# Performance work log

Measured on AMD Instinct MI355X. Metric: run time of the kernel, lower is better.

Reference implementation:

```python
import jax, jax.numpy as jnp
import numpy as np

B, S, D, H = 2, 2048, 1024, 16
HD = D // H  # head_dim = 64
ROPE_BASE = 10000.0
NEG = -1e9


def rope_cos_sin(seq_len, head_dim, dtype):
    inv_freq = 1.0 / (ROPE_BASE ** (jnp.arange(0, head_dim, 2, dtype=jnp.float32) / head_dim))
    t = jnp.arange(seq_len, dtype=jnp.float32)
    freqs = jnp.outer(t, inv_freq)              # [S, HD/2]
    emb = jnp.concatenate([freqs, freqs], axis=-1)  # [S, HD]
    return jnp.cos(emb).astype(dtype), jnp.sin(emb).astype(dtype)


def rotate_half(x):
    half = x.shape[-1] // 2
    return jnp.concatenate([-x[..., half:], x[..., :half]], axis=-1)


def setup_inputs() -> dict:
    key = jax.random.key(0)
    ks = jax.random.split(key, 9)
    s = 0.02
    x = jax.random.normal(ks[0], (B, S, D), dtype=jnp.float32)
    # additive causal mask: 0 on/below diagonal, -1e9 above
    mask = jnp.where(jnp.tril(jnp.ones((S, S), dtype=bool)), 0.0, NEG).astype(jnp.float32)
    params = {
        'Wq': jax.random.normal(ks[1], (D, D), jnp.float32) * s,
        'bq': jnp.zeros((D,), jnp.float32),
        'Wk': jax.random.normal(ks[2], (D, D), jnp.float32) * s,
        'bk': jnp.zeros((D,), jnp.float32),
        'Wv': jax.random.normal(ks[3], (D, D), jnp.float32) * s,
        'bv': jnp.zeros((D,), jnp.float32),
        'Wo': jax.random.normal(ks[4], (D, D), jnp.float32) * s,
        'bo': jnp.zeros((D,), jnp.float32),
    }
    return {'x': x, 'mask': mask, **params}


def reference(x, mask, Wq, bq, Wk, bk, Wv, bv, Wo, bo):
    Bv, Sv, Dv = x.shape
    q = (x @ Wq + bq).reshape(Bv, Sv, H, HD).transpose(0, 2, 1, 3)  # [B,H,S,HD]
    k = (x @ Wk + bk).reshape(Bv, Sv, H, HD).transpose(0, 2, 1, 3)
    v = (x @ Wv + bv).reshape(Bv, Sv, H, HD).transpose(0, 2, 1, 3)
    cos, sin = rope_cos_sin(Sv, HD, x.dtype)      # [S, HD]
    cos = cos[None, None]                          # [1,1,S,HD]
    sin = sin[None, None]
    q = q * cos + rotate_half(q) * sin
    k = k * cos + rotate_half(k) * sin
    scale = jnp.asarray(np.sqrt(HD), x.dtype)
    scores = jnp.einsum('bhqd,bhkd->bhqk', q, k) / scale  # [B,H,S,S]
    scores = scores + mask[None, None]
    attn = jax.nn.softmax(scores, axis=-1)
    out = jnp.einsum('bhqk,bhkd->bhqd', attn, v)   # [B,H,S,HD]
    out = out.transpose(0, 2, 1, 3).reshape(Bv, Sv, Dv)
    return out @ Wo + bo
```

## Files before the change

kernel.cpp:

```cpp
#include <hip/hip_runtime.h>
#include <hip/hip_bf16.h>
#include <cstdint>

typedef __bf16 bf16;
typedef __bf16 bf16x4 __attribute__((ext_vector_type(4)));
typedef __bf16 bf16x8 __attribute__((ext_vector_type(8)));
typedef float f32x4 __attribute__((ext_vector_type(4)));

#define DEV __device__ __forceinline__

DEV void gl_lds16(const void* g, void* l) {
    __builtin_amdgcn_global_load_lds(
        (__attribute__((address_space(1))) void*)(uintptr_t)g,
        (__attribute__((address_space(3))) void*)(uint32_t)(uintptr_t)l,
        16, 0, 0);
}

DEV f32x4 mfma16(bf16x8 a, bf16x8 b, f32x4 c) {
    return __builtin_amdgcn_mfma_f32_16x16x32_bf16(a, b, c, 0, 0, 0);
}

__global__ __launch_bounds__(256) void prep_k(
    const float* __restrict__ x, bf16* __restrict__ xb,
    const float* __restrict__ w0, const float* __restrict__ w1,
    const float* __restrict__ w2, const float* __restrict__ w3,
    bf16* __restrict__ WT, float* __restrict__ cosT, float* __restrict__ sinT) {
    __shared__ float t[32][33];
    const int blk = (int)blockIdx.x;
    const int tid = threadIdx.x;
    if (blk < 4096) {
        const int i = blk * 256 + tid;
        const float4 v = ((const float4*)x)[i];
        bf16x4 o = {(bf16)v.x, (bf16)v.y, (bf16)v.z, (bf16)v.w};
        *(bf16x4*)(xb + (size_t)i * 4) = o;
    } else if (blk < 8192) {
        const int j = blk - 4096;
        const int z = j >> 10, jy = (j >> 5) & 31, jx = j & 31;
        const float* W = z == 0 ? w0 : z == 1 ? w1 : z == 2 ? w2 : w3;
        bf16* dst = WT + (size_t)z * 1024 * 1024;
        const int tx = tid & 31, ty = tid >> 5;
        const int kb = jx * 32, nb = jy * 32;
#pragma unroll
        for (int i = 0; i < 4; ++i)
            t[ty + i * 8][tx] = W[(size_t)(kb + ty + i * 8) * 1024 + nb + tx];
        __syncthreads();
#pragma unroll
        for (int i = 0; i < 4; ++i)
            dst[(size_t)(nb + ty + i * 8) * 1024 + kb + tx] = (bf16)t[tx][ty + i * 8];
    } else {
        const int tt = (blk - 8192) * 256 + tid;
        const int s = tt >> 6, i = tt & 31;
        const float inv = expf(-(float)i * (9.210340371976184f / 32.0f));
        const float ang = (float)s * inv;
        cosT[tt] = cosf(ang);
        sinT[tt] = sinf(ang);
    }
}

__global__ __launch_bounds__(512, 1) void gemm256_k(
    const bf16* __restrict__ A, const bf16* __restrict__ BT,
    const float* __restrict__ bq, const float* __restrict__ bk,
    const float* __restrict__ bv,
    bf16* __restrict__ outQ, bf16* __restrict__ outK, bf16* __restrict__ outV,
    const float* __restrict__ cosT, const float* __restrict__ sinT) {
    extern __shared__ char smem[];
    const int tid = threadIdx.x;
    const int lane = tid & 63, wv = tid >> 6;
    const int wm2 = wv >> 2, wn2 = wv & 3;
    const int q = lane & 15, g = lane >> 4;

    const int gid = (int)blockIdx.x;
    const int xcd = gid & 7, idx = gid >> 3;
    const int bm = (xcd & 3) * 4 + (idx & 3);
    const int bn = (xcd >> 2) * 6 + (idx >> 2);

    const bf16* Ab = A + (size_t)bm * 256 * 1024;
    const bf16* Bb = BT + (size_t)bn * 256 * 1024;

    auto stage = [&](int b, int kb) {
        char* base = smem + b * 65536;
#pragma unroll
        for (int i = 0; i < 4; ++i) {
            const int Xs = i * 8192 + tid * 16;
            const int row = Xs >> 7;
            const int cb = (Xs & 127) ^ ((row & 7) << 4);
            gl_lds16(Ab + (size_t)row * 1024 + kb + (cb >> 1), base + Xs);
        }
#pragma unroll
        for (int i = 0; i < 4; ++i) {
            const int Xs = i * 8192 + tid * 16;
            const int row = Xs >> 7;
            const int cb = (Xs & 127) ^ ((row & 7) << 4);
            gl_lds16(Bb + (size_t)row * 1024 + kb + (cb >> 1), base + 32768 + Xs);
        }
    };

    f32x4 acc[8][4] = {};

    stage(0, 0);

    for (int t = 0; t < 16; ++t) {
        asm volatile("s_waitcnt vmcnt(0)" ::: "memory");
        __builtin_amdgcn_s_barrier();
        if (t + 1 < 16) stage((t + 1) & 1, (t + 1) * 64);
        const char* cbuf = smem + (t & 1) * 65536;
        bf16x8 bfr[4];
#pragma unroll
        for (int p = 0; p < 4; ++p) {
            const int ks = p >> 1, mih = p & 1;
            if (mih == 0) {
#pragma unroll
                for (int ni = 0; ni < 4; ++ni) {
                    const int row = wn2 * 64 + ni * 16 + q;
                    bfr[ni] = *(const bf16x8*)(cbuf + 32768 + row * 128 +
                                               ((ks * 64 + g * 16) ^ ((q & 7) << 4)));
                }
            }
            bf16x8 af[4];
#pragma unroll
            for (int j = 0; j < 4; ++j) {
                const int row = wm2 * 128 + (mih * 4 + j) * 16 + q;
                af[j] = *(const bf16x8*)(cbuf + row * 128 +
                                         ((ks * 64 + g * 16) ^ ((q & 7) << 4)));
            }
            __builtin_amdgcn_s_setprio(1);
#pragma unroll
            for (int j = 0; j < 4; ++j)
#pragma unroll
                for (int ni = 0; ni < 4; ++ni)
                    acc[mih * 4 + j][ni] = mfma16(af[j], bfr[ni], acc[mih * 4 + j][ni]);
            __builtin_amdgcn_s_setprio(0);
        }
    }

    const int n0 = bn * 256 + wn2 * 64;
    const int seg = n0 >> 10;
    const int nloc = n0 & 1023;
    const int h = nloc >> 6;
    const float* bias = seg == 0 ? bq : (seg == 1 ? bk : bv);
    const float qsc = (seg == 0) ? 0.125f : 1.0f;
    float bvv[4];
#pragma unroll
    for (int ni = 0; ni < 4; ++ni) bvv[ni] = bias[nloc + ni * 16 + q];

    if (seg < 2) {
        bf16* dst = seg == 0 ? outQ : outK;
#pragma unroll
        for (int mi = 0; mi < 8; ++mi) {
#pragma unroll
            for (int r = 0; r < 4; ++r) {
                const int m = bm * 256 + wm2 * 128 + mi * 16 + g * 4 + r;
                const int s = m & 2047, bb = m >> 11;
                const size_t rowb = ((size_t)((bb << 4) | h) * 2048 + s) * 64;
#pragma unroll
                for (int ni = 0; ni < 4; ++ni) {
                    const int hd = ni * 16 + q;
                    const float c = cosT[s * 64 + hd], sn = sinT[s * 64 + hd];
                    const float v0 = acc[mi][ni][r] + bvv[ni];
                    const float v1 = acc[mi][ni ^ 2][r] + bvv[ni ^ 2];
                    dst[rowb + hd] = (bf16)((v0 * c + (ni < 2 ? -v1 : v1) * sn) * qsc);
                }
            }
        }
    } else {
        __builtin_amdgcn_s_barrier();
        bf16* Tw = (bf16*)smem + wv * (64 * 72);
        const int bb = (bm * 256) >> 11;
        bf16* vbase = outV + (size_t)((bb << 4) | h) * (64 * 2048);
#pragma unroll
        for (int sh = 0; sh < 2; ++sh) {
#pragma unroll
            for (int mi2 = 0; mi2 < 4; ++mi2)
#pragma unroll
                for (int ni = 0; ni < 4; ++ni)
#pragma unroll
                    for (int r = 0; r < 4; ++r)
                        Tw[(ni * 16 + q) * 72 + mi2 * 16 + g * 4 + r] =
                            (bf16)(acc[sh * 4 + mi2][ni][r] + bvv[ni]);
            const int s0 = ((bm * 256) & 2047) + wm2 * 128 + sh * 64;
#pragma unroll
            for (int i = 0; i < 8; ++i) {
                const int row = i * 8 + (lane >> 3);
                const int col = (lane & 7) * 8;
                bf16x8 vvv = *(const bf16x8*)(Tw + row * 72 + col);
                *(bf16x8*)(vbase + (size_t)row * 2048 + s0 + col) = vvv;
            }
        }
    }
}

__global__ __launch_bounds__(256) void gemmo_k(
    const bf16* __restrict__ A, const bf16* __restrict__ BT,
    const float* __restrict__ bias0, float* __restrict__ outF) {
    extern __shared__ char smem[];
    const int tid = threadIdx.x;
    const int lane = tid & 63;
    const int wv = tid >> 6;
    const int wm = wv >> 1, wn = wv & 1;
    const int bm = blockIdx.x, bn = blockIdx.y;
    const int q = lane & 15, g = lane >> 4;

    const bf16* Ab = A + (size_t)bm * 128 * 1024;
    const bf16* Bb = BT + (size_t)bn * 128 * 1024;
    const int r0 = tid >> 2, c0 = (tid & 3) * 8;

    auto stage = [&](int b, int kb) {
        char* base = smem + b * 16384;
        gl_lds16(Ab + (size_t)r0 * 1024 + kb + c0, base + tid * 16);
        gl_lds16(Ab + (size_t)(r0 + 64) * 1024 + kb + c0, base + 4096 + tid * 16);
        gl_lds16(Bb + (size_t)r0 * 1024 + kb + c0, base + 8192 + tid * 16);
        gl_lds16(Bb + (size_t)(r0 + 64) * 1024 + kb + c0, base + 12288 + tid * 16);
    };

    f32x4 acc[4][4] = {};

    stage(0, 0);
    stage(1, 32);
    asm volatile("s_waitcnt vmcnt(4)" ::: "memory");
    __builtin_amdgcn_s_barrier();

    for (int kt = 0; kt < 32; ++kt) {
        if (kt + 2 < 32) stage((kt + 2) % 3, (kt + 2) * 32);
        const bf16* As = (const bf16*)(smem + (kt % 3) * 16384);
        const bf16* Bs = As + 128 * 32;
        bf16x8 af[4], bfr[4];
#pragma unroll
        for (int mi = 0; mi < 4; ++mi)
            af[mi] = *(const bf16x8*)(As + (wm * 64 + mi * 16 + q) * 32 + g * 8);
#pragma unroll
        for (int ni = 0; ni < 4; ++ni)
            bfr[ni] = *(const bf16x8*)(Bs + (wn * 64 + ni * 16 + q) * 32 + g * 8);
#pragma unroll
        for (int mi = 0; mi < 4; ++mi)
#pragma unroll
            for (int ni = 0; ni < 4; ++ni)
                acc[mi][ni] = mfma16(af[mi], bfr[ni], acc[mi][ni]);
        if (kt + 2 < 32) asm volatile("s_waitcnt vmcnt(4)" ::: "memory");
        else             asm volatile("s_waitcnt vmcnt(0)" ::: "memory");
        __builtin_amdgcn_s_barrier();
    }

    const int n0 = bn * 128 + wn * 64;
    float bvv[4];
#pragma unroll
    for (int ni = 0; ni < 4; ++ni) bvv[ni] = bias0[n0 + ni * 16 + q];
#pragma unroll
    for (int mi = 0; mi < 4; ++mi)
#pragma unroll
        for (int r = 0; r < 4; ++r) {
            const int m = bm * 128 + wm * 64 + mi * 16 + g * 4 + r;
#pragma unroll
            for (int ni = 0; ni < 4; ++ni)
                outF[(size_t)m * 1024 + n0 + ni * 16 + q] = acc[mi][ni][r] + bvv[ni];
        }
}

__global__ __launch_bounds__(512, 2) void attn_k(const bf16* __restrict__ Qr,
                                                 const bf16* __restrict__ Kr,
                                                 const bf16* __restrict__ Vt,
                                                 bf16* __restrict__ AO) {
    const int gid = (int)blockIdx.x;
    const int xcd = gid & 7;
    const int bh = xcd + 8 * ((gid >> 3) & 3);
    const int idx = gid >> 5;
    const int p = idx >> 1;
    const int h = 1 - (idx & 1);
    const int tid = threadIdx.x;
    const int lane = tid & 63, wv = tid >> 6;
    const int q = lane & 15, g = lane >> 4;
    const int qt_w = (wv >> 2) ? p : (15 - p);
    const int q0w = qt_w * 128 + h * 64 + (wv & 3) * 16;
    const int nt = 31 - 2 * p + h;
    const size_t hb = (size_t)bh * (2048 * 64);
    extern __shared__ char smem[];
    bf16* P = (bf16*)(smem + 49152 + wv * 2304);

    const bf16* Kg = Kr + hb;
    const bf16* Vg = Vt + hb;
    const int swz = (q & 7) << 4;

    auto stage = [&](int b, int kb) {
        char* base = smem + b * 16384;
        {
            const int X = tid * 16;
            const int row = X >> 7;
            const int cbg = (X & 127) ^ ((row & 7) << 4);
            gl_lds16(Kg + (size_t)(kb + row) * 64 + (cbg >> 1), base + X);
        }
        {
            const int X = tid * 16;
            const int row = X >> 7;
            const int cbg = (X & 127) ^ ((row & 7) << 4);
            gl_lds16(Vg + (size_t)row * 2048 + kb + (cbg >> 1), base + 8192 + X);
        }
    };

    bf16x8 qf[2];
    {
        const bf16* qp = Qr + hb + (size_t)(q0w + q) * 64 + g * 8;
        qf[0] = *(const bf16x8*)(qp);
        qf[1] = *(const bf16x8*)(qp + 32);
    }
    f32x4 o[4] = {};
    float l_run = 0.0f;
    const f32x4 z4 = {0.f, 0.f, 0.f, 0.f};
    const int rmax = q0w + 15;

    stage(0, 0);
    stage(1, 64);
    asm volatile("s_waitcnt vmcnt(2)" ::: "memory");
    __builtin_amdgcn_s_barrier();

    for (int kt = 0; kt < nt; ++kt) {
        const int kb = kt * 64;
        if (kt + 2 < nt) stage((kt + 2) % 3, kb + 128);
        if (kb <= rmax) {
            char* Kl = smem + (kt % 3) * 16384;
            char* Vl = Kl + 8192;
            f32x4 st[4];
            __builtin_amdgcn_s_setprio(1);
#pragma unroll
            for (int f = 0; f < 4; ++f) {
                const int row = f * 16 + q;
                const bf16x8 k0 = *(const bf16x8*)(Kl + row * 128 + ((g * 16) ^ swz));
                const bf16x8 k1 = *(const bf16x8*)(Kl + row * 128 + ((64 + g * 16) ^ swz));
                f32x4 t0 = mfma16(k0, qf[0], z4);
                st[f] = mfma16(k1, qf[1], t0);
            }
            __builtin_amdgcn_s_setprio(0);
            bf16x8 vf[4][2];
#pragma unroll
            for (int nf = 0; nf < 4; ++nf) {
                const int row = nf * 16 + q;
                vf[nf][0] = *(const bf16x8*)(Vl + row * 128 + ((g * 16) ^ swz));
                vf[nf][1] = *(const bf16x8*)(Vl + row * 128 + ((64 + g * 16) ^ swz));
            }
            float tsum = 0.f;
            if (kb + 63 > q0w) {
#pragma unroll
                for (int f = 0; f < 4; ++f)
#pragma unroll
                    for (int r = 0; r < 4; ++r) {
                        float sv = st[f][r];
                        if (kb + f * 16 + g * 4 + r > q0w + q) sv = -3.0e38f;
                        const float pv = __expf(fminf(sv, 20.0f));
                        st[f][r] = pv;
                        tsum += pv;
                    }
            } else {
#pragma unroll
                for (int f = 0; f < 4; ++f)
#pragma unroll
                    for (int r = 0; r < 4; ++r) {
                        const float pv = __expf(fminf(st[f][r], 20.0f));
                        st[f][r] = pv;
                        tsum += pv;
                    }
            }
            l_run += tsum;
#pragma unroll
            for (int f = 0; f < 4; ++f) {
                bf16x4 pv = {(bf16)st[f][0], (bf16)st[f][1],
                             (bf16)st[f][2], (bf16)st[f][3]};
                *(bf16x4*)&P[q * 72 + f * 16 + g * 4] = pv;
            }
            __builtin_amdgcn_s_setprio(1);
#pragma unroll
            for (int t = 0; t < 2; ++t) {
                const bf16x8 pa = *(const bf16x8*)&P[q * 72 + t * 32 + g * 8];
#pragma unroll
                for (int nf = 0; nf < 4; ++nf)
                    o[nf] = mfma16(pa, vf[nf][t], o[nf]);
            }
            __builtin_amdgcn_s_setprio(0);
        }
        if (kt + 2 < nt) asm volatile("s_waitcnt vmcnt(2)" ::: "memory");
        else             asm volatile("s_waitcnt vmcnt(0)" ::: "memory");
        __builtin_amdgcn_s_barrier();
    }

    l_run += __shfl_xor(l_run, 16);
    l_run += __shfl_xor(l_run, 32);
    float li[4];
#pragma unroll
    for (int r = 0; r < 4; ++r) li[r] = 1.0f / __shfl(l_run, g * 4 + r);
    const int b_ = bh >> 4, h_ = bh & 15;
#pragma unroll
    for (int nf = 0; nf < 4; ++nf)
#pragma unroll
        for (int r = 0; r < 4; ++r) {
            const int qg = q0w + g * 4 + r;
            AO[(size_t)(b_ * 2048 + qg) * 1024 + h_ * 64 + nf * 16 + q] =
                (bf16)(o[nf][r] * li[r]);
        }
}


extern "C" void kernel_launch(void* const* d_in, const int* in_sizes, int n_in,
                              void* d_out, int out_size, void* d_ws, size_t ws_size,
                              hipStream_t stream) {
    const float* x  = (const float*)d_in[0];
    const float* Wq = (const float*)d_in[2];
    const float* bq = (const float*)d_in[3];
    const float* Wk = (const float*)d_in[4];
    const float* bk = (const float*)d_in[5];
    const float* Wv = (const float*)d_in[6];
    const float* bv = (const float*)d_in[7];
    const float* Wo = (const float*)d_in[8];
    const float* bo = (const float*)d_in[9];
    float* out = (float*)d_out;
    char* ws = (char*)d_ws;
    const size_t MB_ = 1024 * 1024;
    bf16* xb    = (bf16*)(ws);
    bf16* WT    = (bf16*)(ws + 8 * MB_);
    bf16* Qrp   = (bf16*)(ws + 16 * MB_);
    bf16* Krp   = (bf16*)(ws + 24 * MB_);
    bf16* Vt    = (bf16*)(ws + 32 * MB_);
    bf16* AO    = (bf16*)(ws + 40 * MB_);
    float* cosT = (float*)(ws + 48 * MB_);
    float* sinT = (float*)(ws + 48 * MB_ + 512 * 1024);

    hipFuncSetAttribute((const void*)gemm256_k,
                        hipFuncAttributeMaxDynamicSharedMemorySize, 131072);

    prep_k<<<8704, 256, 0, stream>>>(x, xb, Wq, Wk, Wv, Wo, WT, cosT, sinT);
    gemm256_k<<<dim3(192), 512, 131072, stream>>>(xb, WT, bq, bk, bv,
                                                  Qrp, Krp, Vt, cosT, sinT);
    attn_k<<<dim3(512, 1), 512, 67584, stream>>>(Qrp, Krp, Vt, AO);
    gemmo_k<<<dim3(32, 8), 256, 49152, stream>>>(AO, WT + (size_t)3072 * 1024, bo, out);
}
```

Measured before the change: 97.30 us.

## Split KV tile across wave halves in attention and merge partial sums

The attention kernel now gives each block a single 64-row query tile, so the grid doubles to 1024 blocks. The two groups of four waves each process half of every 64-key tile and combine their partial outputs and row sums through shared memory at the end. This replaces the earlier pairing of a light and a heavy causal query tile per block, with the aim of more parallelism and less per-wave work per key tile. The cost is heavier load imbalance across blocks (ordered longest first), a shared-memory merge step with an extra barrier, and only half the waves doing the final writes.

```diff
diff --git a/kernel.cpp b/kernel.cpp
--- a/kernel.cpp
+++ b/kernel.cpp
@@ -262,18 +262,16 @@
     const int gid = (int)blockIdx.x;
     const int xcd = gid & 7;
     const int bh = xcd + 8 * ((gid >> 3) & 3);
-    const int idx = gid >> 5;
-    const int p = idx >> 1;
-    const int h = 1 - (idx & 1);
+    const int j = 31 - (gid >> 5);
     const int tid = threadIdx.x;
     const int lane = tid & 63, wv = tid >> 6;
     const int q = lane & 15, g = lane >> 4;
-    const int qt_w = (wv >> 2) ? p : (15 - p);
-    const int q0w = qt_w * 128 + h * 64 + (wv & 3) * 16;
-    const int nt = 31 - 2 * p + h;
+    const int half = wv >> 2;
+    const int q0w = j * 64 + (wv & 3) * 16;
+    const int nt = j + 1;
     const size_t hb = (size_t)bh * (2048 * 64);
     extern __shared__ char smem[];
-    bf16* P = (bf16*)(smem + 49152 + wv * 2304);
+    bf16* P = (bf16*)(smem + 49152 + wv * 1280);
 
     const bf16* Kg = Kr + hb;
     const bf16* Vg = Vt + hb;
@@ -307,49 +305,49 @@
     const int rmax = q0w + 15;
 
     stage(0, 0);
-    stage(1, 64);
+    if (nt > 1) stage(1, 64);
     asm volatile("s_waitcnt vmcnt(2)" ::: "memory");
     __builtin_amdgcn_s_barrier();
 
     for (int kt = 0; kt < nt; ++kt) {
         const int kb = kt * 64;
         if (kt + 2 < nt) stage((kt + 2) % 3, kb + 128);
-        if (kb <= rmax) {
+        const int kvb = kb + half * 32;
+        if (kvb <= rmax) {
             char* Kl = smem + (kt % 3) * 16384;
             char* Vl = Kl + 8192;
-            f32x4 st[4];
+            f32x4 st[2];
             __builtin_amdgcn_s_setprio(1);
 #pragma unroll
-            for (int f = 0; f < 4; ++f) {
-                const int row = f * 16 + q;
+            for (int f = 0; f < 2; ++f) {
+                const int row = half * 32 + f * 16 + q;
                 const bf16x8 k0 = *(const bf16x8*)(Kl + row * 128 + ((g * 16) ^ swz));
                 const bf16x8 k1 = *(const bf16x8*)(Kl + row * 128 + ((64 + g * 16) ^ swz));
                 f32x4 t0 = mfma16(k0, qf[0], z4);
                 st[f] = mfma16(k1, qf[1], t0);
             }
             __builtin_amdgcn_s_setprio(0);
-            bf16x8 vf[4][2];
+            bf16x8 vf[4];
 #pragma unroll
             for (int nf = 0; nf < 4; ++nf) {
                 const int row = nf * 16 + q;
-                vf[nf][0] = *(const bf16x8*)(Vl + row * 128 + ((g * 16) ^ swz));
-                vf[nf][1] = *(const bf16x8*)(Vl + row * 128 + ((64 + g * 16) ^ swz));
+                vf[nf] = *(const bf16x8*)(Vl + row * 128 + ((half * 64 + g * 16) ^ swz));
             }
             float tsum = 0.f;
-            if (kb + 63 > q0w) {
-#pragma unroll
-                for (int f = 0; f < 4; ++f)
+            if (kvb + 31 > q0w) {
+#pragma unroll
+                for (int f = 0; f < 2; ++f)
 #pragma unroll
                     for (int r = 0; r < 4; ++r) {
                         float sv = st[f][r];
-                        if (kb + f * 16 + g * 4 + r > q0w + q) sv = -3.0e38f;
+                        if (kvb + f * 16 + g * 4 + r > q0w + q) sv = -3.0e38f;
                         const float pv = __expf(fminf(sv, 20.0f));
                         st[f][r] = pv;
                         tsum += pv;
                     }
             } else {
 #pragma unroll
-                for (int f = 0; f < 4; ++f)
+                for (int f = 0; f < 2; ++f)
 #pragma unroll
                     for (int r = 0; r < 4; ++r) {
                         const float pv = __expf(fminf(st[f][r], 20.0f));
@@ -359,18 +357,17 @@
             }
             l_run += tsum;
 #pragma unroll
-            for (int f = 0; f < 4; ++f) {
+            for (int f = 0; f < 2; ++f) {
                 bf16x4 pv = {(bf16)st[f][0], (bf16)st[f][1],
                              (bf16)st[f][2], (bf16)st[f][3]};
-                *(bf16x4*)&P[q * 72 + f * 16 + g * 4] = pv;
+                *(bf16x4*)&P[q * 40 + f * 16 + g * 4] = pv;
             }
             __builtin_amdgcn_s_setprio(1);
-#pragma unroll
-            for (int t = 0; t < 2; ++t) {
-                const bf16x8 pa = *(const bf16x8*)&P[q * 72 + t * 32 + g * 8];
+            {
+                const bf16x8 pa = *(const bf16x8*)&P[q * 40 + g * 8];
 #pragma unroll
                 for (int nf = 0; nf < 4; ++nf)
-                    o[nf] = mfma16(pa, vf[nf][t], o[nf]);
+                    o[nf] = mfma16(pa, vf[nf], o[nf]);
             }
             __builtin_amdgcn_s_setprio(0);
         }
@@ -379,20 +376,36 @@
         __builtin_amdgcn_s_barrier();
     }
 
-    l_run += __shfl_xor(l_run, 16);
-    l_run += __shfl_xor(l_run, 32);
-    float li[4];
-#pragma unroll
-    for (int r = 0; r < 4; ++r) li[r] = 1.0f / __shfl(l_run, g * 4 + r);
-    const int b_ = bh >> 4, h_ = bh & 15;
-#pragma unroll
-    for (int nf = 0; nf < 4; ++nf)
-#pragma unroll
-        for (int r = 0; r < 4; ++r) {
-            const int qg = q0w + g * 4 + r;
-            AO[(size_t)(b_ * 2048 + qg) * 1024 + h_ * 64 + nf * 16 + q] =
-                (bf16)(o[nf][r] * li[r]);
-        }
+    float* mrg = (float*)(smem + (wv & 3) * 4352);
+    if (half) {
+#pragma unroll
+        for (int nf = 0; nf < 4; ++nf)
+#pragma unroll
+            for (int r = 0; r < 4; ++r) mrg[(nf * 4 + r) * 64 + lane] = o[nf][r];
+        mrg[16 * 64 + lane] = l_run;
+    }
+    __builtin_amdgcn_s_barrier();
+    if (!half) {
+#pragma unroll
+        for (int nf = 0; nf < 4; ++nf)
+#pragma unroll
+            for (int r = 0; r < 4; ++r) o[nf][r] += mrg[(nf * 4 + r) * 64 + lane];
+        l_run += mrg[16 * 64 + lane];
+        l_run += __shfl_xor(l_run, 16);
+        l_run += __shfl_xor(l_run, 32);
+        float li[4];
+#pragma unroll
+        for (int r = 0; r < 4; ++r) li[r] = 1.0f / __shfl(l_run, g * 4 + r);
+        const int b_ = bh >> 4, h_ = bh & 15;
+#pragma unroll
+        for (int nf = 0; nf < 4; ++nf)
+#pragma unroll
+            for (int r = 0; r < 4; ++r) {
+                const int qg = q0w + g * 4 + r;
+                AO[(size_t)(b_ * 2048 + qg) * 1024 + h_ * 64 + nf * 16 + q] =
+                    (bf16)(o[nf][r] * li[r]);
+            }
+    }
 }
 
 
@@ -426,6 +439,6 @@
     prep_k<<<8704, 256, 0, stream>>>(x, xb, Wq, Wk, Wv, Wo, WT, cosT, sinT);
     gemm256_k<<<dim3(192), 512, 131072, stream>>>(xb, WT, bq, bk, bv,
                                                   Qrp, Krp, Vt, cosT, sinT);
-    attn_k<<<dim3(512, 1), 512, 67584, stream>>>(Qrp, Krp, Vt, AO);
+    attn_k<<<dim3(1024, 1), 512, 59392, stream>>>(Qrp, Krp, Vt, AO);
     gemmo_k<<<dim3(32, 8), 256, 49152, stream>>>(AO, WT + (size_t)3072 * 1024, bo, out);
 }
```

Measured after the change: 101.7 us. 1.04x slower.

## Use 16 waves per block in QKV GEMM and fold log2e into Q scale

Applied to the files above, without the earlier changes.

The fused QKV projection GEMM now launches 1024 threads (16 waves) per 256x256 tile. Each wave owns a 64x64 sub-tile, which halves the per-wave accumulator count. The V transpose epilogue runs in two barrier-separated rounds so the LDS scratch space still fits. Separately, the Q scale now includes log2(e), so the attention softmax can call exp2f directly instead of __expf, with the clamp constant adjusted to match. The aim is more latency hiding in the GEMM and fewer multiplies in the softmax. The cost is more LDS read traffic per MFMA and an extra barrier in the epilogue.

```diff
diff --git a/kernel.cpp b/kernel.cpp
--- a/kernel.cpp
+++ b/kernel.cpp
@@ -57,7 +57,7 @@
     }
 }
 
-__global__ __launch_bounds__(512, 1) void gemm256_k(
+__global__ __launch_bounds__(1024, 1) void gemm256_k(
     const bf16* __restrict__ A, const bf16* __restrict__ BT,
     const float* __restrict__ bq, const float* __restrict__ bk,
     const float* __restrict__ bv,
@@ -66,7 +66,7 @@
     extern __shared__ char smem[];
     const int tid = threadIdx.x;
     const int lane = tid & 63, wv = tid >> 6;
-    const int wm2 = wv >> 2, wn2 = wv & 3;
+    const int wm3 = wv >> 2, wn3 = wv & 3;
     const int q = lane & 15, g = lane >> 4;
 
     const int gid = (int)blockIdx.x;
@@ -80,22 +80,22 @@
     auto stage = [&](int b, int kb) {
         char* base = smem + b * 65536;
 #pragma unroll
-        for (int i = 0; i < 4; ++i) {
-            const int Xs = i * 8192 + tid * 16;
+        for (int i = 0; i < 2; ++i) {
+            const int Xs = i * 16384 + tid * 16;
             const int row = Xs >> 7;
             const int cb = (Xs & 127) ^ ((row & 7) << 4);
             gl_lds16(Ab + (size_t)row * 1024 + kb + (cb >> 1), base + Xs);
         }
 #pragma unroll
-        for (int i = 0; i < 4; ++i) {
-            const int Xs = i * 8192 + tid * 16;
+        for (int i = 0; i < 2; ++i) {
+            const int Xs = i * 16384 + tid * 16;
             const int row = Xs >> 7;
             const int cb = (Xs & 127) ^ ((row & 7) << 4);
             gl_lds16(Bb + (size_t)row * 1024 + kb + (cb >> 1), base + 32768 + Xs);
         }
     };
 
-    f32x4 acc[8][4] = {};
+    f32x4 acc[4][4] = {};
 
     stage(0, 0);
 
@@ -104,22 +104,18 @@
         __builtin_amdgcn_s_barrier();
         if (t + 1 < 16) stage((t + 1) & 1, (t + 1) * 64);
         const char* cbuf = smem + (t & 1) * 65536;
-        bf16x8 bfr[4];
-#pragma unroll
-        for (int p = 0; p < 4; ++p) {
-            const int ks = p >> 1, mih = p & 1;
-            if (mih == 0) {
-#pragma unroll
-                for (int ni = 0; ni < 4; ++ni) {
-                    const int row = wn2 * 64 + ni * 16 + q;
-                    bfr[ni] = *(const bf16x8*)(cbuf + 32768 + row * 128 +
-                                               ((ks * 64 + g * 16) ^ ((q & 7) << 4)));
-                }
-            }
-            bf16x8 af[4];
+#pragma unroll
+        for (int ks = 0; ks < 2; ++ks) {
+            bf16x8 bfr[4], af[4];
+#pragma unroll
+            for (int ni = 0; ni < 4; ++ni) {
+                const int row = wn3 * 64 + ni * 16 + q;
+                bfr[ni] = *(const bf16x8*)(cbuf + 32768 + row * 128 +
+                                           ((ks * 64 + g * 16) ^ ((q & 7) << 4)));
+            }
 #pragma unroll
             for (int j = 0; j < 4; ++j) {
-                const int row = wm2 * 128 + (mih * 4 + j) * 16 + q;
+                const int row = wm3 * 64 + j * 16 + q;
                 af[j] = *(const bf16x8*)(cbuf + row * 128 +
                                          ((ks * 64 + g * 16) ^ ((q & 7) << 4)));
             }
@@ -128,17 +124,17 @@
             for (int j = 0; j < 4; ++j)
 #pragma unroll
                 for (int ni = 0; ni < 4; ++ni)
-                    acc[mih * 4 + j][ni] = mfma16(af[j], bfr[ni], acc[mih * 4 + j][ni]);
+                    acc[j][ni] = mfma16(af[j], bfr[ni], acc[j][ni]);
             __builtin_amdgcn_s_setprio(0);
         }
     }
 
-    const int n0 = bn * 256 + wn2 * 64;
+    const int n0 = bn * 256 + wn3 * 64;
     const int seg = n0 >> 10;
     const int nloc = n0 & 1023;
     const int h = nloc >> 6;
     const float* bias = seg == 0 ? bq : (seg == 1 ? bk : bv);
-    const float qsc = (seg == 0) ? 0.125f : 1.0f;
+    const float qsc = (seg == 0) ? 0.18033688f : 1.0f;
     float bvv[4];
 #pragma unroll
     for (int ni = 0; ni < 4; ++ni) bvv[ni] = bias[nloc + ni * 16 + q];
@@ -146,10 +142,10 @@
     if (seg < 2) {
         bf16* dst = seg == 0 ? outQ : outK;
 #pragma unroll
-        for (int mi = 0; mi < 8; ++mi) {
+        for (int mi = 0; mi < 4; ++mi) {
 #pragma unroll
             for (int r = 0; r < 4; ++r) {
-                const int m = bm * 256 + wm2 * 128 + mi * 16 + g * 4 + r;
+                const int m = bm * 256 + wm3 * 64 + mi * 16 + g * 4 + r;
                 const int s = m & 2047, bb = m >> 11;
                 const size_t rowb = ((size_t)((bb << 4) | h) * 2048 + s) * 64;
 #pragma unroll
@@ -163,27 +159,29 @@
             }
         }
     } else {
-        __builtin_amdgcn_s_barrier();
-        bf16* Tw = (bf16*)smem + wv * (64 * 72);
         const int bb = (bm * 256) >> 11;
         bf16* vbase = outV + (size_t)((bb << 4) | h) * (64 * 2048);
-#pragma unroll
-        for (int sh = 0; sh < 2; ++sh) {
-#pragma unroll
-            for (int mi2 = 0; mi2 < 4; ++mi2)
-#pragma unroll
-                for (int ni = 0; ni < 4; ++ni)
-#pragma unroll
-                    for (int r = 0; r < 4; ++r)
-                        Tw[(ni * 16 + q) * 72 + mi2 * 16 + g * 4 + r] =
-                            (bf16)(acc[sh * 4 + mi2][ni][r] + bvv[ni]);
-            const int s0 = ((bm * 256) & 2047) + wm2 * 128 + sh * 64;
-#pragma unroll
-            for (int i = 0; i < 8; ++i) {
-                const int row = i * 8 + (lane >> 3);
-                const int col = (lane & 7) * 8;
-                bf16x8 vvv = *(const bf16x8*)(Tw + row * 72 + col);
-                *(bf16x8*)(vbase + (size_t)row * 2048 + s0 + col) = vvv;
+        const int s0 = ((bm * 256) & 2047) + wm3 * 64;
+#pragma unroll
+        for (int rnd = 0; rnd < 2; ++rnd) {
+            __builtin_amdgcn_s_barrier();
+            if ((wv >> 3) == rnd) {
+                bf16* Tw = (bf16*)smem + (wv & 7) * (64 * 72);
+#pragma unroll
+                for (int mi2 = 0; mi2 < 4; ++mi2)
+#pragma unroll
+                    for (int ni = 0; ni < 4; ++ni)
+#pragma unroll
+                        for (int r = 0; r < 4; ++r)
+                            Tw[(ni * 16 + q) * 72 + mi2 * 16 + g * 4 + r] =
+                                (bf16)(acc[mi2][ni][r] + bvv[ni]);
+#pragma unroll
+                for (int i = 0; i < 8; ++i) {
+                    const int row = i * 8 + (lane >> 3);
+                    const int col = (lane & 7) * 8;
+                    bf16x8 vvv = *(const bf16x8*)(Tw + row * 72 + col);
+                    *(bf16x8*)(vbase + (size_t)row * 2048 + s0 + col) = vvv;
+                }
             }
         }
     }
@@ -343,7 +341,7 @@
                     for (int r = 0; r < 4; ++r) {
                         float sv = st[f][r];
                         if (kb + f * 16 + g * 4 + r > q0w + q) sv = -3.0e38f;
-                        const float pv = __expf(fminf(sv, 20.0f));
+                        const float pv = exp2f(fminf(sv, 28.853901f));
                         st[f][r] = pv;
                         tsum += pv;
                     }
@@ -352,7 +350,7 @@
                 for (int f = 0; f < 4; ++f)
 #pragma unroll
                     for (int r = 0; r < 4; ++r) {
-                        const float pv = __expf(fminf(st[f][r], 20.0f));
+                        const float pv = exp2f(fminf(st[f][r], 28.853901f));
                         st[f][r] = pv;
                         tsum += pv;
                     }
@@ -424,8 +422,8 @@
                         hipFuncAttributeMaxDynamicSharedMemorySize, 131072);
 
     prep_k<<<8704, 256, 0, stream>>>(x, xb, Wq, Wk, Wv, Wo, WT, cosT, sinT);
-    gemm256_k<<<dim3(192), 512, 131072, stream>>>(xb, WT, bq, bk, bv,
-                                                  Qrp, Krp, Vt, cosT, sinT);
+    gemm256_k<<<dim3(192), 1024, 131072, stream>>>(xb, WT, bq, bk, bv,
+                                                   Qrp, Krp, Vt, cosT, sinT);
     attn_k<<<dim3(512, 1), 512, 67584, stream>>>(Qrp, Krp, Vt, AO);
     gemmo_k<<<dim3(32, 8), 256, 49152, stream>>>(AO, WT + (size_t)3072 * 1024, bo, out);
 }
```

Result: slower. 100.6 us (+3.4%).
